# Optimization experiments

Measured on AMD Instinct MI355X. Metric: run time of the kernel, lower is better.

Reference implementation:

```python
import jax, jax.numpy as jnp
import numpy as np

N, E, G = 2048, 65536, 32
F_ATOM, LAT, IN, ED, NB, L = 16, 64, 128, 32, 5, 5


def setup_inputs() -> dict:
    key = jax.random.key(0)
    ks = iter(jax.random.split(key, 64))
    nxt = lambda: next(ks)
    def w(shape):
        fan_in = shape[-2] if len(shape) >= 2 else 1
        return jax.random.normal(nxt(), shape, jnp.float32) / np.sqrt(fan_in)
    inp = {}
    inp['x'] = jax.random.normal(nxt(), (N, F_ATOM), jnp.float32)
    inp['t'] = jax.random.uniform(nxt(), (G, 1), jnp.float32)
    inp['z'] = jax.random.normal(nxt(), (N, LAT), jnp.float32)
    inp['edge_index'] = jax.random.randint(nxt(), (2, E), 0, N, jnp.int32)
    inp['edge_attr'] = jax.random.normal(nxt(), (E, NB), jnp.float32)
    inp['batch'] = jnp.sort(jax.random.randint(nxt(), (N,), 0, G, jnp.int32))
    inp['batch_edge_global'] = jax.random.randint(nxt(), (E,), 0, G, jnp.int32)
    # top-level dense layers
    inp['Wt_a'] = w((1, IN)); inp['bt_a'] = jnp.zeros((IN,))
    inp['Wt_b'] = w((1, ED)); inp['bt_b'] = jnp.zeros((ED,))
    inp['W_atom'] = w((F_ATOM, IN)); inp['b_atom'] = jnp.zeros((IN,))
    inp['W_bond'] = w((NB, ED)); inp['b_bond'] = jnp.zeros((ED,))
    inp['W_lat'] = w((LAT, IN)); inp['b_lat'] = jnp.zeros((IN,))
    inp['W_at'] = w((IN, IN)); inp['b_at'] = jnp.zeros((IN,))
    inp['W_bt'] = w((ED, ED)); inp['b_bt'] = jnp.zeros((ED,))
    # TopoEdgeGNN: L layers of edge-conditioned message passing with edge update
    inp['Wmsg'] = w((L, 2 * IN + ED, IN)); inp['bmsg'] = jnp.zeros((L, IN))
    inp['Wnode'] = w((L, 2 * IN, IN)); inp['bnode'] = jnp.zeros((L, IN))
    inp['Wedge'] = w((L, 2 * IN + ED, ED)); inp['bedge'] = jnp.zeros((L, ED))
    # prediction head
    inp['Wsh'] = w((IN, IN)); inp['bsh'] = jnp.zeros((IN,))
    inp['Wbm'] = w((ED, IN)); inp['bbm'] = jnp.zeros((IN,))
    inp['Wbl'] = w((IN, NB)); inp['bbl'] = jnp.zeros((NB,))
    inp['Wal'] = w((IN, F_ATOM + LAT)); inp['bal'] = jnp.zeros((F_ATOM + LAT,))
    return inp


def reference(x, t, z, edge_index, edge_attr, batch, batch_edge_global,
              Wt_a, bt_a, Wt_b, bt_b, W_atom, b_atom, W_bond, b_bond,
              W_lat, b_lat, W_at, b_at, W_bt, b_bt,
              Wmsg, bmsg, Wnode, bnode, Wedge, bedge,
              Wsh, bsh, Wbm, bbm, Wbl, bbl, Wal, bal):
    j, i = edge_index[0], edge_index[1]
    # time embeddings, gathered to nodes / edges
    ta = t @ Wt_a + bt_a            # [G, IN]
    tb = t @ Wt_b + bt_b            # [G, ED]
    tnode = ta[batch]               # [N, IN]
    tedge = tb[batch_edge_global]   # [E, ED]
    # node features
    s = x @ W_atom + b_atom
    s = (s + tnode) @ W_at + b_at
    s = s + (z @ W_lat + b_lat)
    # edge features
    e = edge_attr @ W_bond + b_bond
    e = (e + tedge) @ W_bt + b_bt
    # TopoEdgeGNN: message passing with residual node/edge updates
    for l in range(L):
        m = jax.nn.silu(jnp.concatenate([s[i], s[j], e], -1) @ Wmsg[l] + bmsg[l])  # [E, IN]
        agg = jax.ops.segment_sum(m, i, num_segments=N)                            # [N, IN]
        s = s + jax.nn.silu(jnp.concatenate([s, agg], -1) @ Wnode[l] + bnode[l])
        e = e + jax.nn.silu(jnp.concatenate([s[i], s[j], e], -1) @ Wedge[l] + bedge[l])
    # prediction head
    s2 = jax.nn.silu(s @ Wsh + bsh)
    al = s2 @ Wal + bal
    atoms_pred, latent_pred = al[:, :F_ATOM], al[:, F_ATOM:]
    # dense edge symmetrization: scatter edges into [N, N, ED], symmetrize, gather back
    e_dense = jnp.zeros((N, N, ED), e.dtype).at[j, i].set(e)
    e_dense = 0.5 * (e_dense + e_dense.transpose(1, 0, 2))
    e_sym = e_dense[j, i]           # [E, ED]
    f = jax.nn.silu(s2[i] + s2[j] + (e_sym @ Wbm + bbm))
    bonds_pred = f @ Wbl + bbl
    return latent_pred, atoms_pred, bonds_pred
```

## Files before the change

### kernel.cpp

```cpp
#include <hip/hip_runtime.h>
#include <hip/hip_bf16.h>

#define NN 2048
#define NE 65536
#define NG 32
#define CIN 128
#define CED 32
#define CLAT 64
#define CFA 16
#define CNB 5
#define NL 5

#define OFF_AT (NN * CLAT)
#define OFF_B  (NN * CLAT + NN * CFA)

typedef __attribute__((ext_vector_type(8))) short bf16x8;
typedef __attribute__((ext_vector_type(4))) float f32x4;

__device__ __forceinline__ float silu_f(float v) { return v / (1.0f + __expf(-v)); }
__device__ __forceinline__ short f2bs(float v) {
    __hip_bfloat16 h = __float2bfloat16(v);
    return *reinterpret_cast<short*>(&h);
}
__device__ __forceinline__ float bs2f(short s) {
    return __bfloat162float(*reinterpret_cast<__hip_bfloat16*>(&s));
}
__device__ __forceinline__ unsigned pack2(float a, float b) {
    return ((unsigned)(unsigned short)f2bs(b) << 16) | (unsigned short)f2bs(a);
}

struct KArgs {
    const float *x, *t, *z;
    const int *jj, *ii;
    const float *ea;
    const int *batch, *beg;
    const float *Wt_a, *bt_a, *Wt_b, *bt_b, *W_atom, *b_atom, *W_bond, *b_bond;
    const float *W_lat, *b_lat, *W_at, *b_at, *W_bt, *b_bt;
    const float *Wmsg, *bmsg, *Wnode, *bnode, *Wedge, *bedge;
    const float *Wsh, *bsh, *Wbm, *bbm, *Wbl, *bbl, *Wal, *bal;
    float *s, *e, *agg;
    int *cnt, *rowpos, *invp, *i_s, *j_s;
    float *s2, *U, *V, *P, *Q;
    int *map;
    short *Wpn, *Wpsh, *Wpal, *Wpbm, *Wproj, *W3m, *We3;
    int *gsync;
    float *out;
};

__device__ __forceinline__ void gbar(int* bar, int* gen, int nb)
{
    __threadfence();
    __syncthreads();
    if (threadIdx.x == 0) {
        int g = __hip_atomic_load(gen, __ATOMIC_RELAXED, __HIP_MEMORY_SCOPE_AGENT);
        if (__hip_atomic_fetch_add(bar, 1, __ATOMIC_ACQ_REL, __HIP_MEMORY_SCOPE_AGENT) == nb - 1) {
            __hip_atomic_store(bar, 0, __ATOMIC_RELAXED, __HIP_MEMORY_SCOPE_AGENT);
            __hip_atomic_store(gen, g + 1, __ATOMIC_RELEASE, __HIP_MEMORY_SCOPE_AGENT);
        } else {
            while (__hip_atomic_load(gen, __ATOMIC_ACQUIRE, __HIP_MEMORY_SCOPE_AGENT) == g)
                __builtin_amdgcn_s_sleep(2);
        }
    }
    __syncthreads();
    __threadfence();
}

__device__ __forceinline__ void phase_pack(const KArgs& a, int start, int stride)
{
    for (int idx = start; idx < 6 * 4 * 20 * 64 * 8; idx += stride) {
        int j = idx & 7, t0 = idx >> 3, lane = t0 & 63, tt = t0 >> 6;
        int kq = (lane >> 4) * 8 + j, n16 = lane & 15;
        if (idx < NL * 8 * 8 * 64 * 8) {
            int nt = tt & 7, kt = (tt >> 3) & 7, l = tt >> 6;
            a.Wpn[idx] = f2bs(a.Wnode[((size_t)l * 256 + kt * 32 + kq) * CIN + nt * 16 + n16]);
        }
        if (idx < 4 * 8 * 64 * 8) {
            int nt = tt & 7, kt = tt >> 3;
            a.Wpsh[idx] = f2bs(a.Wsh[(size_t)(kt * 32 + kq) * CIN + nt * 16 + n16]);
        }
        if (idx < 4 * 5 * 64 * 8) {
            int nt = tt % 5, kt = tt / 5;
            a.Wpal[idx] = f2bs(a.Wal[(size_t)(kt * 32 + kq) * 80 + nt * 16 + n16]);
        }
        if (idx < 8 * 64 * 8) {
            int nt = tt & 7;
            a.Wpbm[idx] = f2bs(a.Wbm[(size_t)kq * CIN + nt * 16 + n16]);
        }
        {
            int nt = tt % 20; int t2 = tt / 20; int kt = t2 & 3; int slot = t2 >> 2;
            int k = kt * 32 + kq;
            float v;
            if (nt < 16) {
                int msgl = slot % 5;
                int srcK = (nt < 8) ? k : 128 + k;
                int col = (nt & 7) * 16 + n16;
                v = a.Wmsg[((size_t)msgl * 288 + srcK) * CIN + col];
            } else {
                int edgel = (slot == 0) ? 0 : slot - 1;
                int srcK = (nt < 18) ? k : 128 + k;
                int col = (nt & 1) * 16 + n16;
                v = a.Wedge[((size_t)edgel * 288 + srcK) * CED + col];
            }
            a.Wproj[idx] = f2bs(v);
        }
        if (idx < NL * 8 * 64 * 8) {
            int nt = tt & 7, l = tt >> 3;
            a.W3m[idx] = f2bs(a.Wmsg[((size_t)l * 288 + 256 + kq) * CIN + nt * 16 + n16]);
        }
        if (idx < NL * 2 * 64 * 8) {
            int nt = tt & 1, l = tt >> 1;
            a.We3[idx] = f2bs(a.Wedge[((size_t)l * 288 + 256 + kq) * CED + nt * 16 + n16]);
        }
    }
}

__device__ __forceinline__ void phase_init_s(const KArgs& a, char* smem, int tile, int tid)
{
    float* xs  = (float*)smem;
    float* zs  = (float*)(smem + 1024);
    float* tmp = (float*)(smem + 5120);
    float* tv  = (float*)(smem + 13312);
    int nb0 = tile * 16;
    int c = tid & 127, h = tid >> 7;
    if (tid < 16 * CFA / 4) ((float4*)xs)[tid] = ((const float4*)a.x)[nb0 * (CFA / 4) + tid];
    if (tid < 16 * CLAT / 4) ((float4*)zs)[tid] = ((const float4*)a.z)[nb0 * (CLAT / 4) + tid];
    if (tid < 16) tv[tid] = a.t[a.batch[nb0 + tid]];
    __syncthreads();
    float wta = a.Wt_a[c], base0 = a.b_atom[c] + a.bt_a[c];
    float acc[8];
#pragma unroll
    for (int q = 0; q < 8; q++) acc[q] = base0 + tv[h * 8 + q] * wta;
    for (int k = 0; k < CFA; k++) {
        float w = a.W_atom[k * CIN + c];
#pragma unroll
        for (int q = 0; q < 8; q++) acc[q] += xs[(h * 8 + q) * CFA + k] * w;
    }
#pragma unroll
    for (int q = 0; q < 8; q++) tmp[(h * 8 + q) * CIN + c] = acc[q];
    __syncthreads();
    float base1 = a.b_at[c] + a.b_lat[c];
    float acc2[8];
#pragma unroll
    for (int q = 0; q < 8; q++) acc2[q] = base1;
    for (int k4 = 0; k4 < CIN / 4; k4++) {
        float w0 = a.W_at[(4 * k4 + 0) * CIN + c], w1 = a.W_at[(4 * k4 + 1) * CIN + c];
        float w2 = a.W_at[(4 * k4 + 2) * CIN + c], w3 = a.W_at[(4 * k4 + 3) * CIN + c];
#pragma unroll
        for (int q = 0; q < 8; q++) {
            float4 f = *(const float4*)&tmp[(h * 8 + q) * CIN + 4 * k4];
            acc2[q] += f.x * w0 + f.y * w1 + f.z * w2 + f.w * w3;
        }
    }
    for (int k4 = 0; k4 < CLAT / 4; k4++) {
        float w0 = a.W_lat[(4 * k4 + 0) * CIN + c], w1 = a.W_lat[(4 * k4 + 1) * CIN + c];
        float w2 = a.W_lat[(4 * k4 + 2) * CIN + c], w3 = a.W_lat[(4 * k4 + 3) * CIN + c];
#pragma unroll
        for (int q = 0; q < 8; q++) {
            float4 f = *(const float4*)&zs[(h * 8 + q) * CLAT + 4 * k4];
            acc2[q] += f.x * w0 + f.y * w1 + f.z * w2 + f.w * w3;
        }
    }
#pragma unroll
    for (int q = 0; q < 8; q++) {
        int nd = nb0 + h * 8 + q;
        a.s[(size_t)nd * CIN + c] = acc2[q];
    }
}

__device__ __forceinline__ void phase_init_e(const KArgs& a, char* smem, int tb, int tid)
{
    float* eas   = (float*)smem;
    float* tv    = (float*)(smem + 1280);
    int*   sp    = (int*)(smem + 1536);
    float* tmp   = (float*)(smem + 1792);
    float* wbt   = (float*)(smem + 10240);
    float* wbond = (float*)(smem + 14336);
    float* cb    = (float*)(smem + 14976);
    float* wtb   = (float*)(smem + 15104);
    float* bbt2  = (float*)(smem + 15232);
    int k0 = tb * 64;
    for (int idx = tid; idx < 320; idx += 256) eas[idx] = a.ea[(size_t)k0 * 5 + idx];
    if (tid < 64) { tv[tid] = a.t[a.beg[k0 + tid]]; sp[tid] = a.invp[k0 + tid]; }
    for (int idx = tid; idx < 1024; idx += 256) wbt[idx] = a.W_bt[idx];
    if (tid < 160) wbond[tid] = a.W_bond[tid];
    if (tid < 32) { cb[tid] = a.b_bond[tid] + a.bt_b[tid]; wtb[tid] = a.Wt_b[tid]; bbt2[tid] = a.b_bt[tid]; }
    __syncthreads();
    int ch = tid & 31, eg = tid >> 5;
#pragma unroll
    for (int q = 0; q < 8; q++) {
        int le = eg * 8 + q;
        float acc = cb[ch] + tv[le] * wtb[ch];
#pragma unroll
        for (int bb = 0; bb < CNB; bb++) acc += eas[le * 5 + bb] * wbond[bb * 32 + ch];
        tmp[le * 33 + ch] = acc;
    }
    __syncthreads();
#pragma unroll
    for (int q = 0; q < 8; q++) {
        int le = eg * 8 + q;
        float acc2 = bbt2[ch];
        for (int d = 0; d < 32; d++) acc2 += tmp[le * 33 + d] * wbt[d * 32 + ch];
        size_t ix = (size_t)sp[le] * CED + ch;
        a.e[ix] = acc2;
        if (ch == 0) {
            int k = k0 + le;
            atomicMax(&a.map[(size_t)a.jj[k] * NN + a.ii[k]], k);
        }
    }
}

__device__ __forceinline__ void phase_node2(
    const KArgs& a, char* smem, int tile, int tid, bool DO_NODE, bool DO_POST,
    bool LOAD_S, bool STORE_S,
    const short* Wpn_l, const float* bnode_l, const short* Wproj_slot, float (*s_reg)[4])
{
    short* feat  = (short*)smem;
    short* feat2 = (short*)(smem + 8448);
    int nb0 = tile * 16;
    int lane = tid & 63, w = tid >> 6;
    int quad = lane >> 4, n16 = lane & 15;

    if (DO_NODE) {
#pragma unroll
        for (int n2 = 0; n2 < 2; n2++) {
            int col = (w * 2 + n2) * 16 + n16;
#pragma unroll
            for (int r = 0; r < 4; r++) {
                int row = quad * 4 + r;
                if (LOAD_S) s_reg[n2][r] = a.s[(size_t)(nb0 + row) * CIN + col];
                feat[row * 264 + col] = f2bs(s_reg[n2][r]);
            }
        }
        for (int idx = tid; idx < 16 * 32; idx += 256) {
            int kl = idx >> 5, c = idx & 31;
            size_t gix = (size_t)(nb0 + kl) * 32 + c;
            float4 v = ((const float4*)a.agg)[gix];
            ((float4*)a.agg)[gix] = (float4){0.f, 0.f, 0.f, 0.f};
            uint2 p; p.x = pack2(v.x, v.y); p.y = pack2(v.z, v.w);
            *(uint2*)&feat[kl * 264 + 128 + 4 * c] = p;
        }
        __syncthreads();
        f32x4 acc[2];
        acc[0] = (f32x4){0.f, 0.f, 0.f, 0.f};
        acc[1] = (f32x4){0.f, 0.f, 0.f, 0.f};
        const short* fbase = feat + n16 * 264 + quad * 8;
#pragma unroll
        for (int kt = 0; kt < 8; kt++) {
            bf16x8 av = *(const bf16x8*)(fbase + kt * 32);
#pragma unroll
            for (int n2 = 0; n2 < 2; n2++) {
                int nt = w * 2 + n2;
                bf16x8 b = *(const bf16x8*)(Wpn_l + ((size_t)(kt * 8 + nt) * 64 + lane) * 8);
                acc[n2] = __builtin_amdgcn_mfma_f32_16x16x32_bf16(av, b, acc[n2], 0, 0, 0);
            }
        }
#pragma unroll
        for (int n2 = 0; n2 < 2; n2++) {
            int col = (w * 2 + n2) * 16 + n16;
            float bb = bnode_l[col];
#pragma unroll
            for (int r = 0; r < 4; r++) {
                int row = quad * 4 + r;
                float v = s_reg[n2][r] + silu_f(acc[n2][r] + bb);
                s_reg[n2][r] = v;
                if (STORE_S) a.s[(size_t)(nb0 + row) * CIN + col] = v;
                feat2[row * 136 + col] = f2bs(v);
            }
        }
        __syncthreads();
    } else {
        int kl = tid >> 4, c = tid & 15;
        const float4* sp4 = (const float4*)&a.s[(size_t)(nb0 + kl) * CIN + c * 8];
        float4 v0 = sp4[0], v1 = sp4[1];
        uint4 p; p.x = pack2(v0.x, v0.y); p.y = pack2(v0.z, v0.w);
        p.z = pack2(v1.x, v1.y); p.w = pack2(v1.z, v1.w);
        *(uint4*)&feat2[kl * 136 + c * 8] = p;
        __syncthreads();
    }

    {
        f32x4 accp[5];
#pragma unroll
        for (int t2 = 0; t2 < 5; t2++) accp[t2] = (f32x4){0.f, 0.f, 0.f, 0.f};
        const short* abase = feat2 + n16 * 136 + quad * 8;
#pragma unroll
        for (int kt = 0; kt < 4; kt++) {
            bf16x8 av = *(const bf16x8*)(abase + kt * 32);
#pragma unroll
            for (int n5 = 0; n5 < 5; n5++) {
                int nt = w * 5 + n5;
                bf16x8 b = *(const bf16x8*)(Wproj_slot + ((size_t)(kt * 20 + nt) * 64 + lane) * 8);
                accp[n5] = __builtin_amdgcn_mfma_f32_16x16x32_bf16(av, b, accp[n5], 0, 0, 0);
            }
        }
#pragma unroll
        for (int n5 = 0; n5 < 5; n5++) {
            int nt = w * 5 + n5;
#pragma unroll
            for (int r = 0; r < 4; r++) {
                int node = tile * 16 + quad * 4 + r;
                float v = accp[n5][r];
                if (nt < 8)       a.U[(size_t)node * CIN + nt * 16 + n16] = v;
                else if (nt < 16) a.V[(size_t)node * CIN + (nt - 8) * 16 + n16] = v;
                else if (nt < 18) a.P[(size_t)node * CED + (nt - 16) * 16 + n16] = v;
                else              a.Q[(size_t)node * CED + (nt - 18) * 16 + n16] = v;
            }
        }
    }

    if (DO_POST) {
        short* feat_s2 = feat;
        const short* fbase = feat2 + n16 * 136 + quad * 8;
        f32x4 acc[2];
        acc[0] = (f32x4){0.f, 0.f, 0.f, 0.f};
        acc[1] = (f32x4){0.f, 0.f, 0.f, 0.f};
#pragma unroll
        for (int kt = 0; kt < 4; kt++) {
            bf16x8 av = *(const bf16x8*)(fbase + kt * 32);
#pragma unroll
            for (int n2 = 0; n2 < 2; n2++) {
                int nt = w * 2 + n2;
                bf16x8 b = *(const bf16x8*)(a.Wpsh + ((size_t)(kt * 8 + nt) * 64 + lane) * 8);
                acc[n2] = __builtin_amdgcn_mfma_f32_16x16x32_bf16(av, b, acc[n2], 0, 0, 0);
            }
        }
#pragma unroll
        for (int n2 = 0; n2 < 2; n2++) {
            int col = (w * 2 + n2) * 16 + n16;
            float bb = a.bsh[col];
#pragma unroll
            for (int r = 0; r < 4; r++) {
                int row = quad * 4 + r;
                float v = silu_f(acc[n2][r] + bb);
                a.s2[(size_t)(nb0 + row) * CIN + col] = v;
                feat_s2[row * 136 + col] = f2bs(v);
            }
        }
        __syncthreads();
        const short* abase2 = feat_s2 + n16 * 136 + quad * 8;
        f32x4 acca[2];
        acca[0] = (f32x4){0.f, 0.f, 0.f, 0.f};
        acca[1] = (f32x4){0.f, 0.f, 0.f, 0.f};
        int nAl = (w == 0) ? 2 : 1;
        int ntl[2] = {w, 4};
#pragma unroll
        for (int kt = 0; kt < 4; kt++) {
            bf16x8 av = *(const bf16x8*)(abase2 + kt * 32);
#pragma unroll
            for (int q = 0; q < 2; q++) {
                if (q < nAl) {
                    bf16x8 b = *(const bf16x8*)(a.Wpal + ((size_t)(kt * 5 + ntl[q]) * 64 + lane) * 8);
                    acca[q] = __builtin_amdgcn_mfma_f32_16x16x32_bf16(av, b, acca[q], 0, 0, 0);
                }
            }
        }
#pragma unroll
        for (int q = 0; q < 2; q++) {
            if (q < nAl) {
                int col = ntl[q] * 16 + n16;
                float bb = a.bal[col];
#pragma unroll
                for (int r = 0; r < 4; r++) {
                    int node = nb0 + quad * 4 + r;
                    float v = acca[q][r] + bb;
                    if (col < CFA) a.out[OFF_AT + node * CFA + col] = v;
                    else           a.out[(size_t)node * CLAT + (col - CFA)] = v;
                }
            }
        }
    }
}

__device__ __forceinline__ void phase_em2(
    const KArgs& a, char* smem, int tb, int tid, bool DO_EDGE, bool DO_MSG, bool LOAD_E, bool WRITE_E,
    const short* We3p, const float* bedge_l, const short* W3mp, const float* bmsg_l,
    float (*e_reg)[4])
{
    short* feat_e = (short*)smem;
    short* uv_bf  = (short*)(smem + 5120);
    short* pq_bf  = (short*)(smem + 22528);
    int*   sii    = (int*)(smem + 27648);
    int*   sjj    = (int*)(smem + 27904);
    int e0 = tb * 64;
    int lane = tid & 63, w = tid >> 6;
    int quad = lane >> 4, n16 = lane & 15;
    if (tid < 64) sii[tid] = a.i_s[e0 + tid];
    else if (tid < 128) sjj[tid - 64] = a.j_s[e0 + tid - 64];
    __syncthreads();
#pragma unroll
    for (int nt = 0; nt < 2; nt++) {
        int ch = nt * 16 + n16;
#pragma unroll
        for (int r = 0; r < 4; r++) {
            int el = w * 16 + quad * 4 + r;
            if (LOAD_E) e_reg[nt][r] = a.e[(size_t)(e0 + el) * CED + ch];
            feat_e[el * 40 + ch] = f2bs(e_reg[nt][r]);
        }
    }
    if (DO_EDGE) {
        for (int idx = tid; idx < 64 * 8; idx += 256) {
            int kl = idx >> 3, c = idx & 7;
            float4 av = ((const float4*)a.P)[(size_t)sii[kl] * 8 + c];
            float4 bv = ((const float4*)a.Q)[(size_t)sjj[kl] * 8 + c];
            uint2 p; p.x = pack2(av.x + bv.x, av.y + bv.y); p.y = pack2(av.z + bv.z, av.w + bv.w);
            *(uint2*)&pq_bf[kl * 40 + 4 * c] = p;
        }
    }
    if (DO_MSG) {
        for (int idx = tid; idx < 64 * 32; idx += 256) {
            int kl = idx >> 5, c = idx & 31;
            float4 av = ((const float4*)a.U)[(size_t)sii[kl] * 32 + c];
            float4 bv = ((const float4*)a.V)[(size_t)sjj[kl] * 32 + c];
            uint2 p; p.x = pack2(av.x + bv.x, av.y + bv.y); p.y = pack2(av.z + bv.z, av.w + bv.w);
            *(uint2*)&uv_bf[kl * 136 + 4 * c] = p;
        }
    }
    __syncthreads();
    const short* abase = feat_e + (w * 16 + n16) * 40 + quad * 8;
    bf16x8 av = *(const bf16x8*)abase;

    if (DO_EDGE) {
        f32x4 acc_e[2];
        acc_e[0] = (f32x4){0.f, 0.f, 0.f, 0.f};
        acc_e[1] = (f32x4){0.f, 0.f, 0.f, 0.f};
#pragma unroll
        for (int nt = 0; nt < 2; nt++) {
            bf16x8 b = *(const bf16x8*)(We3p + ((size_t)(nt * 64 + lane)) * 8);
            acc_e[nt] = __builtin_amdgcn_mfma_f32_16x16x32_bf16(av, b, acc_e[nt], 0, 0, 0);
        }
#pragma unroll
        for (int nt = 0; nt < 2; nt++) {
            int ch = nt * 16 + n16;
            float bb = bedge_l[ch];
#pragma unroll
            for (int r = 0; r < 4; r++) {
                int el = w * 16 + quad * 4 + r;
                float v = e_reg[nt][r] + silu_f(acc_e[nt][r] + bb + bs2f(pq_bf[el * 40 + ch]));
                e_reg[nt][r] = v;
                feat_e[el * 40 + ch] = f2bs(v);
                if (WRITE_E) a.e[(size_t)(e0 + el) * CED + ch] = v;
            }
        }
        av = *(const bf16x8*)abase;
    }

    if (DO_MSG) {
        f32x4 acc_m[8];
#pragma unroll
        for (int t2 = 0; t2 < 8; t2++) acc_m[t2] = (f32x4){0.f, 0.f, 0.f, 0.f};
#pragma unroll
        for (int nt = 0; nt < 8; nt++) {
            bf16x8 b = *(const bf16x8*)(W3mp + ((size_t)(nt * 64 + lane)) * 8);
            acc_m[nt] = __builtin_amdgcn_mfma_f32_16x16x32_bf16(av, b, acc_m[nt], 0, 0, 0);
        }
#pragma unroll
        for (int nt = 0; nt < 8; nt++) {
            int ch = nt * 16 + n16;
            float bb = bmsg_l[ch];
#pragma unroll
            for (int r = 0; r < 4; r++) {
                int el = w * 16 + quad * 4 + r;
                int lix = el * 136 + ch;
                float m = silu_f(acc_m[nt][r] + bb + bs2f(uv_bf[lix]));
                uv_bf[lix] = f2bs(m);
            }
        }
        __syncthreads();
        if (tid < 128) {
            int c = tid;
            float run = 0.f;
            int cur = sii[0];
            for (int r = 0; r < 64; r++) {
                int tg = sii[r];
                if (tg != cur) { atomicAdd(&a.agg[(size_t)cur * CIN + c], run); run = 0.f; cur = tg; }
                run += bs2f(uv_bf[r * 136 + c]);
            }
            atomicAdd(&a.agg[(size_t)cur * CIN + c], run);
        }
    }
}

__device__ __forceinline__ void phase_post_edge(const KArgs& a, char* smem, int tb, int tid)
{
    short* esym  = (short*)smem;
    short* sbias = (short*)(smem + 5120);
    int* sii = (int*)(smem + 22016);
    int* sjj = (int*)(smem + 22272);
    int* skf = (int*)(smem + 22528);
    int* skb = (int*)(smem + 22784);
    int e0 = tb * 64;
    if (tid < 64) sii[tid] = a.ii[e0 + tid];
    else if (tid < 128) sjj[tid - 64] = a.jj[e0 + tid - 64];
    __syncthreads();
    if (tid < 64) skf[tid] = a.invp[a.map[(size_t)sjj[tid] * NN + sii[tid]]];
    else if (tid < 128) {
        int m = a.map[(size_t)sii[tid - 64] * NN + sjj[tid - 64]];
        skb[tid - 64] = (m >= 0) ? a.invp[m] : -1;
    }
    __syncthreads();
    for (int idx = tid; idx < 64 * 8; idx += 256) {
        int kl = idx >> 3, c = idx & 7;
        float4 av = ((const float4*)a.e)[(size_t)skf[kl] * 8 + c];
        int kb = skb[kl];
        float4 bv = {0.f, 0.f, 0.f, 0.f};
        if (kb >= 0) bv = ((const float4*)a.e)[(size_t)kb * 8 + c];
        uint2 p; p.x = pack2(0.5f * (av.x + bv.x), 0.5f * (av.y + bv.y));
        p.y = pack2(0.5f * (av.z + bv.z), 0.5f * (av.w + bv.w));
        *(uint2*)&esym[kl * 40 + 4 * c] = p;
    }
    for (int idx = tid; idx < 64 * 32; idx += 256) {
        int kl = idx >> 5, c = idx & 31;
        float4 av = ((const float4*)a.s2)[(size_t)sii[kl] * 32 + c];
        float4 bv = ((const float4*)a.s2)[(size_t)sjj[kl] * 32 + c];
        uint2 p; p.x = pack2(av.x + bv.x, av.y + bv.y); p.y = pack2(av.z + bv.z, av.w + bv.w);
        *(uint2*)&sbias[kl * 132 + 4 * c] = p;
    }
    __syncthreads();
    int lane = tid & 63, w = tid >> 6;
    int quad = lane >> 4, n16 = lane & 15;
    bf16x8 av = *(const bf16x8*)(esym + (w * 16 + n16) * 40 + quad * 8);
    f32x4 acc[8];
#pragma unroll
    for (int nt = 0; nt < 8; nt++) {
        bf16x8 b = *(const bf16x8*)(a.Wpbm + ((size_t)nt * 64 + lane) * 8);
        f32x4 zero = {0.f, 0.f, 0.f, 0.f};
        acc[nt] = __builtin_amdgcn_mfma_f32_16x16x32_bf16(av, b, zero, 0, 0, 0);
    }
    float f[8][4];
#pragma unroll
    for (int nt = 0; nt < 8; nt++) {
        int col = nt * 16 + n16;
        float bb = a.bbm[col];
#pragma unroll
        for (int r = 0; r < 4; r++) {
            int row = w * 16 + quad * 4 + r;
            f[nt][r] = silu_f(acc[nt][r] + bb + bs2f(sbias[row * 132 + col]));
        }
    }
    __syncthreads();
    short* fshT = sbias;
#pragma unroll
    for (int nt = 0; nt < 8; nt++) {
        int col = nt * 16 + n16;
#pragma unroll
        for (int r = 0; r < 4; r++) {
            int row = w * 16 + quad * 4 + r;
            fshT[col * 66 + row] = f2bs(f[nt][r]);
        }
    }
    __syncthreads();
    for (int idx = tid; idx < 64 * CNB; idx += 256) {
        int kl = idx / CNB, b = idx - kl * CNB;
        float acc3 = a.bbl[b];
        for (int d = 0; d < CIN; d++) acc3 += bs2f(fshT[d * 66 + kl]) * a.Wbl[d * CNB + b];
        a.out[OFF_B + (size_t)(e0 + kl) * CNB + b] = acc3;
    }
}

__global__ __launch_bounds__(256, 4) void k_main(KArgs a)
{
    __shared__ __align__(16) char smem[28160];
    int bid = blockIdx.x, tid = threadIdx.x;
    int* bar = a.gsync; int* gen = a.gsync + 1;

    a.agg[bid * 256 + tid] = 0.f;
    if (bid < 8) a.cnt[bid * 256 + tid] = 0;
    gbar(bar, gen, 1024);

    if (bid < 128) phase_init_s(a, smem, bid, tid);
    else phase_pack(a, (bid - 128) * 256 + tid, 896 * 256);
    if (bid >= 192 && bid < 448) atomicAdd(&a.cnt[a.ii[(bid - 192) * 256 + tid]], 1);
    {
        int4 m1 = {-1, -1, -1, -1};
#pragma unroll
        for (int q = 0; q < 4; q++)
            ((int4*)a.map)[(size_t)bid * 1024 + q * 256 + tid] = m1;
    }
    gbar(bar, gen, 1024);

    if (bid == 0) {
        int* part = (int*)smem;
        int loc[8], sum = 0;
#pragma unroll
        for (int q = 0; q < 8; q++) { loc[q] = a.cnt[tid * 8 + q]; sum += loc[q]; }
        part[tid] = sum;
        __syncthreads();
        if (tid == 0) { int r = 0; for (int i = 0; i < 256; i++) { int v = part[i]; part[i] = r; r += v; } }
        __syncthreads();
        int r = part[tid];
#pragma unroll
        for (int q = 0; q < 8; q++) { a.rowpos[tid * 8 + q] = r; r += loc[q]; }
    }
    gbar(bar, gen, 1024);

    if (bid < 256) {
        int k = bid * 256 + tid;
        int iv = a.ii[k];
        int p = atomicAdd(&a.rowpos[iv], 1);
        a.invp[k] = p;
        a.i_s[p] = iv;
        a.j_s[p] = a.jj[k];
    }
    gbar(bar, gen, 1024);

    phase_init_e(a, smem, bid, tid);
    gbar(bar, gen, 1024);

    float s_reg[2][4], e_reg[2][4];

    if (bid < 128) phase_node2(a, smem, bid, tid, false, false, false, false,
                               nullptr, nullptr, a.Wproj, s_reg);
    gbar(bar, gen, 1024);

    phase_em2(a, smem, bid, tid, false, true, true, false, nullptr, nullptr, a.W3m, a.bmsg, e_reg);
    gbar(bar, gen, 1024);

    for (int l = 0; l < NL; l++) {
        if (bid < 128)
            phase_node2(a, smem, bid, tid, true, l == NL - 1, l == 0, false,
                        a.Wpn + (size_t)l * 8 * 8 * 64 * 8, a.bnode + l * CIN,
                        a.Wproj + (size_t)(l + 1) * 4 * 20 * 64 * 8, s_reg);
        gbar(bar, gen, 1024);
        bool dm = (l < NL - 1);
        phase_em2(a, smem, bid, tid, true, dm, false, l == NL - 1,
                  a.We3 + (size_t)l * 2 * 64 * 8, a.bedge + l * CED,
                  dm ? a.W3m + (size_t)(l + 1) * 8 * 64 * 8 : a.W3m,
                  dm ? a.bmsg + (l + 1) * CIN : a.bmsg, e_reg);
        gbar(bar, gen, 1024);
    }

    phase_post_edge(a, smem, bid, tid);
}

__global__ __launch_bounds__(256) void k_prologue(KArgs a)
{
    __shared__ __align__(16) char smem[13440];
    int b = blockIdx.x, tid = threadIdx.x;
    if (b < 960) phase_pack(a, b * 256 + tid, 960 * 256);
    else if (b < 1088) phase_init_s(a, smem, b - 960, tid);
    else {
        int base = (b - 1088) * 1024;
#pragma unroll
        for (int q = 0; q < 4; q++) atomicAdd(&a.cnt[a.ii[base + q * 256 + tid]], 1);
    }
}
__global__ __launch_bounds__(256) void k_prefix(KArgs a)
{
    __shared__ int part[256];
    int tid = threadIdx.x;
    int loc[8], sum = 0;
#pragma unroll
    for (int q = 0; q < 8; q++) { loc[q] = a.cnt[tid * 8 + q]; sum += loc[q]; }
    part[tid] = sum;
    __syncthreads();
    if (tid == 0) { int r = 0; for (int i = 0; i < 256; i++) { int v = part[i]; part[i] = r; r += v; } }
    __syncthreads();
    int r = part[tid];
#pragma unroll
    for (int q = 0; q < 8; q++) { a.rowpos[tid * 8 + q] = r; r += loc[q]; }
}
__global__ void k_perm(KArgs a)
{
    int k = blockIdx.x * 256 + threadIdx.x;
    int iv = a.ii[k];
    int p = atomicAdd(&a.rowpos[iv], 1);
    a.invp[k] = p;
    a.i_s[p] = iv;
    a.j_s[p] = a.jj[k];
}
__global__ __launch_bounds__(256) void k_init_e(KArgs a)
{
    __shared__ __align__(16) char smem[15360];
    phase_init_e(a, smem, blockIdx.x, threadIdx.x);
}
__global__ __launch_bounds__(256) void k_node_proj(KArgs a, int donode, int dopost,
                                                   const short* Wpn_l, const float* bnode_l,
                                                   const short* Wproj_slot)
{
    __shared__ __align__(16) char smem[12800];
    float s_reg[2][4];
    phase_node2(a, smem, blockIdx.x, threadIdx.x, donode != 0, dopost != 0,
                donode != 0, donode != 0, Wpn_l, bnode_l, Wproj_slot, s_reg);
}
__global__ __launch_bounds__(256) void k_em(KArgs a, int de, int dm, const short* We3p,
                                            const float* bedge_l, const short* W3mp, const float* bmsg_l)
{
    __shared__ __align__(16) char smem[28160];
    float e_reg[2][4];
    phase_em2(a, smem, blockIdx.x, threadIdx.x, de != 0, dm != 0, true, de != 0,
              We3p, bedge_l, W3mp, bmsg_l, e_reg);
}
__global__ __launch_bounds__(256) void k_post_edge(KArgs a)
{
    __shared__ __align__(16) char smem[23040];
    phase_post_edge(a, smem, blockIdx.x, threadIdx.x);
}

extern "C" void kernel_launch(void* const* d_in, const int* in_sizes, int n_in,
                              void* d_out, int out_size, void* d_ws, size_t ws_size,
                              hipStream_t stream) {
    KArgs a;
    a.x      = (const float*)d_in[0];
    a.t      = (const float*)d_in[1];
    a.z      = (const float*)d_in[2];
    const int* eidx = (const int*)d_in[3];
    a.jj     = eidx;
    a.ii     = eidx + NE;
    a.ea     = (const float*)d_in[4];
    a.batch  = (const int*)d_in[5];
    a.beg    = (const int*)d_in[6];
    a.Wt_a   = (const float*)d_in[7];
    a.bt_a   = (const float*)d_in[8];
    a.Wt_b   = (const float*)d_in[9];
    a.bt_b   = (const float*)d_in[10];
    a.W_atom = (const float*)d_in[11];
    a.b_atom = (const float*)d_in[12];
    a.W_bond = (const float*)d_in[13];
    a.b_bond = (const float*)d_in[14];
    a.W_lat  = (const float*)d_in[15];
    a.b_lat  = (const float*)d_in[16];
    a.W_at   = (const float*)d_in[17];
    a.b_at   = (const float*)d_in[18];
    a.W_bt   = (const float*)d_in[19];
    a.b_bt   = (const float*)d_in[20];
    a.Wmsg   = (const float*)d_in[21];
    a.bmsg   = (const float*)d_in[22];
    a.Wnode  = (const float*)d_in[23];
    a.bnode  = (const float*)d_in[24];
    a.Wedge  = (const float*)d_in[25];
    a.bedge  = (const float*)d_in[26];
    a.Wsh    = (const float*)d_in[27];
    a.bsh    = (const float*)d_in[28];
    a.Wbm    = (const float*)d_in[29];
    a.bbm    = (const float*)d_in[30];
    a.Wbl    = (const float*)d_in[31];
    a.bbl    = (const float*)d_in[32];
    a.Wal    = (const float*)d_in[33];
    a.bal    = (const float*)d_in[34];

    a.s      = (float*)d_ws;
    a.e      = a.s + (size_t)NN * CIN;
    a.agg    = a.e + (size_t)NE * CED;
    a.cnt    = (int*)(a.agg + (size_t)NN * CIN);
    a.rowpos = a.cnt + NN;
    a.invp   = a.rowpos + NN;
    a.i_s    = a.invp + NE;
    a.j_s    = a.i_s + NE;
    a.s2     = (float*)(a.j_s + NE);
    a.U      = a.s2 + (size_t)NN * CIN;
    a.V      = a.U + (size_t)NN * CIN;
    a.P      = a.V + (size_t)NN * CIN;
    a.Q      = a.P + (size_t)NN * CED;
    a.map    = (int*)(a.Q + (size_t)NN * CED);
    a.Wpn    = (short*)(a.map + (size_t)NN * NN);
    a.Wpsh   = a.Wpn + (size_t)NL * 8 * 8 * 64 * 8;
    a.Wpal   = a.Wpsh + (size_t)4 * 8 * 64 * 8;
    a.Wpbm   = a.Wpal + (size_t)4 * 5 * 64 * 8;
    a.Wproj  = a.Wpbm + (size_t)8 * 64 * 8;
    a.W3m    = a.Wproj + (size_t)6 * 4 * 20 * 64 * 8;
    a.We3    = a.W3m + (size_t)NL * 8 * 64 * 8;
    a.gsync  = (int*)(a.We3 + (size_t)NL * 2 * 64 * 8);
    a.out    = (float*)d_out;

    static int use_fused = -1;
    if (use_fused < 0) {
        int dev = 0;
        (void)hipGetDevice(&dev);
        hipDeviceProp_t props;
        int ncu = 0;
        if (hipGetDeviceProperties(&props, dev) == hipSuccess) ncu = props.multiProcessorCount;
        int maxb = 0;
        if (hipOccupancyMaxActiveBlocksPerMultiprocessor(&maxb, k_main, 256, 0) != hipSuccess) maxb = 0;
        use_fused = ((long)maxb * ncu >= 1024) ? 1 : 0;
    }

    if (use_fused) {
        hipMemsetAsync(a.gsync, 0, 2 * sizeof(int), stream);
        k_main<<<1024, 256, 0, stream>>>(a);
    } else {
        hipMemsetAsync(a.map, 0xFF, (size_t)NN * NN * sizeof(int), stream);
        hipMemsetAsync(a.agg, 0, ((size_t)NN * CIN + NN) * sizeof(float), stream);
        k_prologue<<<1152, 256, 0, stream>>>(a);
        k_prefix<<<1, 256, 0, stream>>>(a);
        k_perm<<<NE / 256, 256, 0, stream>>>(a);
        k_init_e<<<NE / 64, 256, 0, stream>>>(a);
        k_node_proj<<<NN / 16, 256, 0, stream>>>(a, 0, 0, nullptr, nullptr, a.Wproj);
        k_em<<<NE / 64, 256, 0, stream>>>(a, 0, 1, nullptr, nullptr, a.W3m, a.bmsg);
        for (int l = 0; l < NL; l++) {
            int dopost = (l == NL - 1) ? 1 : 0;
            k_node_proj<<<NN / 16, 256, 0, stream>>>(a, 1, dopost,
                a.Wpn + (size_t)l * 8 * 8 * 64 * 8, a.bnode + l * CIN,
                a.Wproj + (size_t)(l + 1) * 4 * 20 * 64 * 8);
            int dm = (l < NL - 1) ? 1 : 0;
            k_em<<<NE / 64, 256, 0, stream>>>(a, 1, dm,
                a.We3 + (size_t)l * 2 * 64 * 8, a.bedge + l * CED,
                dm ? a.W3m + (size_t)(l + 1) * 8 * 64 * 8 : a.W3m,
                dm ? a.bmsg + (l + 1) * CIN : a.bmsg);
        }
        k_post_edge<<<NE / 64, 256, 0, stream>>>(a);
    }
}
```

Measured before the change: 355.7 us.

## Use hierarchical grid barrier and drop two barrier phases from fused kernel

Replaces the flat single-counter grid barrier with a two-level barrier: each group of 32 blocks counts on its own padded counter, and the last block of each group bumps a top-level counter that releases a generation flag. This is meant to cut atomic contention on one address across 1024 blocks. The cnt zeroing moves to a host memset so the first barrier can go, and the initial node projection moves into the prefix-scan phase, removing one more barrier. There are now more memsets and an extra level of atomic latency per barrier, and it relies on the node projection not depending on the prefix or permutation phases.

```diff
diff --git a/kernel.cpp b/kernel.cpp
--- a/kernel.cpp
+++ b/kernel.cpp
@@ -47,19 +47,22 @@
     float *out;
 };
 
-__device__ __forceinline__ void gbar(int* bar, int* gen, int nb)
-{
-    __threadfence();
+__device__ __forceinline__ void gbar(int* gs)
+{
     __syncthreads();
     if (threadIdx.x == 0) {
-        int g = __hip_atomic_load(gen, __ATOMIC_RELAXED, __HIP_MEMORY_SCOPE_AGENT);
-        if (__hip_atomic_fetch_add(bar, 1, __ATOMIC_ACQ_REL, __HIP_MEMORY_SCOPE_AGENT) == nb - 1) {
-            __hip_atomic_store(bar, 0, __ATOMIC_RELAXED, __HIP_MEMORY_SCOPE_AGENT);
-            __hip_atomic_store(gen, g + 1, __ATOMIC_RELEASE, __HIP_MEMORY_SCOPE_AGENT);
-        } else {
-            while (__hip_atomic_load(gen, __ATOMIC_ACQUIRE, __HIP_MEMORY_SCOPE_AGENT) == g)
-                __builtin_amdgcn_s_sleep(2);
-        }
+        __threadfence();
+        int g = __hip_atomic_load(gs + 32, __ATOMIC_RELAXED, __HIP_MEMORY_SCOPE_AGENT);
+        int* gc = gs + 64 + ((blockIdx.x >> 5) << 5);
+        if (__hip_atomic_fetch_add(gc, 1, __ATOMIC_ACQ_REL, __HIP_MEMORY_SCOPE_AGENT) == 31) {
+            __hip_atomic_store(gc, 0, __ATOMIC_RELAXED, __HIP_MEMORY_SCOPE_AGENT);
+            if (__hip_atomic_fetch_add(gs, 1, __ATOMIC_ACQ_REL, __HIP_MEMORY_SCOPE_AGENT) == 31) {
+                __hip_atomic_store(gs, 0, __ATOMIC_RELAXED, __HIP_MEMORY_SCOPE_AGENT);
+                __hip_atomic_store(gs + 32, g + 1, __ATOMIC_RELEASE, __HIP_MEMORY_SCOPE_AGENT);
+            }
+        }
+        while (__hip_atomic_load(gs + 32, __ATOMIC_RELAXED, __HIP_MEMORY_SCOPE_AGENT) == g)
+            __builtin_amdgcn_s_sleep(8);
     }
     __syncthreads();
     __threadfence();
@@ -561,12 +564,10 @@
 {
     __shared__ __align__(16) char smem[28160];
     int bid = blockIdx.x, tid = threadIdx.x;
-    int* bar = a.gsync; int* gen = a.gsync + 1;
+    int* gs = a.gsync;
+    float s_reg[2][4], e_reg[2][4];
 
     a.agg[bid * 256 + tid] = 0.f;
-    if (bid < 8) a.cnt[bid * 256 + tid] = 0;
-    gbar(bar, gen, 1024);
-
     if (bid < 128) phase_init_s(a, smem, bid, tid);
     else phase_pack(a, (bid - 128) * 256 + tid, 896 * 256);
     if (bid >= 192 && bid < 448) atomicAdd(&a.cnt[a.ii[(bid - 192) * 256 + tid]], 1);
@@ -576,7 +577,7 @@
         for (int q = 0; q < 4; q++)
             ((int4*)a.map)[(size_t)bid * 1024 + q * 256 + tid] = m1;
     }
-    gbar(bar, gen, 1024);
+    gbar(gs);
 
     if (bid == 0) {
         int* part = (int*)smem;
@@ -590,8 +591,11 @@
         int r = part[tid];
 #pragma unroll
         for (int q = 0; q < 8; q++) { a.rowpos[tid * 8 + q] = r; r += loc[q]; }
-    }
-    gbar(bar, gen, 1024);
+        __syncthreads();
+    }
+    if (bid < 128) phase_node2(a, smem, bid, tid, false, false, false, false,
+                               nullptr, nullptr, a.Wproj, s_reg);
+    gbar(gs);
 
     if (bid < 256) {
         int k = bid * 256 + tid;
@@ -601,32 +605,26 @@
         a.i_s[p] = iv;
         a.j_s[p] = a.jj[k];
     }
-    gbar(bar, gen, 1024);
+    gbar(gs);
 
     phase_init_e(a, smem, bid, tid);
-    gbar(bar, gen, 1024);
-
-    float s_reg[2][4], e_reg[2][4];
-
-    if (bid < 128) phase_node2(a, smem, bid, tid, false, false, false, false,
-                               nullptr, nullptr, a.Wproj, s_reg);
-    gbar(bar, gen, 1024);
+    gbar(gs);
 
     phase_em2(a, smem, bid, tid, false, true, true, false, nullptr, nullptr, a.W3m, a.bmsg, e_reg);
-    gbar(bar, gen, 1024);
+    gbar(gs);
 
     for (int l = 0; l < NL; l++) {
         if (bid < 128)
             phase_node2(a, smem, bid, tid, true, l == NL - 1, l == 0, false,
                         a.Wpn + (size_t)l * 8 * 8 * 64 * 8, a.bnode + l * CIN,
                         a.Wproj + (size_t)(l + 1) * 4 * 20 * 64 * 8, s_reg);
-        gbar(bar, gen, 1024);
+        gbar(gs);
         bool dm = (l < NL - 1);
         phase_em2(a, smem, bid, tid, true, dm, false, l == NL - 1,
                   a.We3 + (size_t)l * 2 * 64 * 8, a.bedge + l * CED,
                   dm ? a.W3m + (size_t)(l + 1) * 8 * 64 * 8 : a.W3m,
                   dm ? a.bmsg + (l + 1) * CIN : a.bmsg, e_reg);
-        gbar(bar, gen, 1024);
+        gbar(gs);
     }
 
     phase_post_edge(a, smem, bid, tid);
@@ -775,7 +773,8 @@
     }
 
     if (use_fused) {
-        hipMemsetAsync(a.gsync, 0, 2 * sizeof(int), stream);
+        hipMemsetAsync(a.gsync, 0, (64 + 32 * 32) * sizeof(int), stream);
+        hipMemsetAsync(a.cnt, 0, NN * sizeof(int), stream);
         k_main<<<1024, 256, 0, stream>>>(a);
     } else {
         hipMemsetAsync(a.map, 0xFF, (size_t)NN * NN * sizeof(int), stream);
```

Result: no change. 356.1 us (+0.1%).
